# Kernel tuning notes

Hardware: AMD Instinct MI355X
Metric: run time of the kernel (lower is better)

Reference implementation:

```python
import jax, jax.numpy as jnp
import numpy as np

NEG_SLOPE = 0.2  # PyG GATConv default


def gat_conv(x, src, dst, W, att_src, att_dst, bias, n_nodes):
    # x: [N, F_in]; W: [F_in, H*C]; att_*: [H, C]; bias: [H*C]
    H, C = att_src.shape
    h = (x @ W).reshape(n_nodes, H, C)                      # [N, H, C]
    a_src = jnp.sum(h * att_src, axis=-1)                   # [N, H]
    a_dst = jnp.sum(h * att_dst, axis=-1)                   # [N, H]
    e = jax.nn.leaky_relu(a_src[src] + a_dst[dst], NEG_SLOPE)  # [E, H]
    # segment softmax over incoming edges of each dst node
    e_max = jax.ops.segment_max(e, dst, num_segments=n_nodes)
    e_max = jnp.where(jnp.isfinite(e_max), e_max, 0.0)
    ex = jnp.exp(e - e_max[dst])                             # [E, H]
    denom = jax.ops.segment_sum(ex, dst, num_segments=n_nodes)
    alpha = ex / (denom[dst] + 1e-16)                        # [E, H]
    msg = h[src] * alpha[:, :, None]                         # [E, H, C]
    out = jax.ops.segment_sum(msg, dst, num_segments=n_nodes)  # [N, H, C]
    return out.reshape(n_nodes, H * C) + bias


def setup_inputs() -> dict:
    key = jax.random.key(0)
    ks = jax.random.split(key, 12)
    N, F_in, Hd, heads, F_out, E = 50000, 128, 32, 8, 16, 800000
    x = jax.random.normal(ks[0], (N, F_in), dtype=jnp.float32)
    edge_index = jax.random.randint(ks[1], (2, E), 0, N, dtype=jnp.int64)
    g = 0.1
    return {
        "x": x,
        "edge_index": edge_index,
        "W1": jax.random.normal(ks[2], (F_in, heads * Hd), dtype=jnp.float32) * g,
        "att_src1": jax.random.normal(ks[3], (heads, Hd), dtype=jnp.float32) * g,
        "att_dst1": jax.random.normal(ks[4], (heads, Hd), dtype=jnp.float32) * g,
        "b1": jnp.zeros((heads * Hd,), dtype=jnp.float32),
        "W2": jax.random.normal(ks[5], (heads * Hd, Hd), dtype=jnp.float32) * g,
        "att_src2": jax.random.normal(ks[6], (1, Hd), dtype=jnp.float32) * g,
        "att_dst2": jax.random.normal(ks[7], (1, Hd), dtype=jnp.float32) * g,
        "b2": jnp.zeros((Hd,), dtype=jnp.float32),
        "Wout": jax.random.normal(ks[8], (Hd, F_out), dtype=jnp.float32) * g,
        "bout": jnp.zeros((F_out,), dtype=jnp.float32),
    }


def reference(x, edge_index, W1, att_src1, att_dst1, b1, W2, att_src2, att_dst2, b2, Wout, bout):
    N = x.shape[0]
    # PyG GATConv adds self loops by default
    loops = jnp.arange(N, dtype=edge_index.dtype)
    src = jnp.concatenate([edge_index[0], loops])
    dst = jnp.concatenate([edge_index[1], loops])
    h = jax.nn.elu(gat_conv(x, src, dst, W1, att_src1, att_dst1, b1, N))
    # dropout is identity in eval mode
    h = jax.nn.elu(gat_conv(h, src, dst, W2, att_src2, att_dst2, b2, N))
    return h @ Wout + bout
```

## Files before the change

kernel.cpp:

```cpp
#include <hip/hip_runtime.h>
#include <math.h>

#define NEG_SLOPE 0.2f

typedef __attribute__((ext_vector_type(8))) short bfrag8;
typedef __attribute__((ext_vector_type(4))) float f4acc;

__device__ __forceinline__ float bflo(unsigned int u) {
  union { unsigned int i; float f; } c;
  c.i = u << 16;
  return c.f;
}
__device__ __forceinline__ float bfhi(unsigned int u) {
  union { unsigned int i; float f; } c;
  c.i = u & 0xFFFF0000u;
  return c.f;
}
__device__ __forceinline__ unsigned short f2bf(float f) {
  union { float f; unsigned int i; } c;
  c.f = f;
  unsigned int i = c.i;
  return (unsigned short)((i + 0x7FFFu + ((i >> 16) & 1u)) >> 16);
}


__global__ __launch_bounds__(256) void hist_kernel(const int* __restrict__ ei,
                                                   int* __restrict__ counts, int e) {
  int i = blockIdx.x * 256 + threadIdx.x;
  if (i < e) atomicAdd(&counts[ei[e + i]], 1);
}

#define SCAN_TILE 2048
__global__ __launch_bounds__(256) void scan1_kernel(const int* __restrict__ counts,
                                                    int* __restrict__ offsets,
                                                    int* __restrict__ bsum, int n) {
  __shared__ int wtot[4];
  int tid = threadIdx.x;
  int base = blockIdx.x * SCAN_TILE + tid * 8;
  int v[8];
#pragma unroll
  for (int k = 0; k < 8; ++k) v[k] = (base + k < n) ? counts[base + k] + 1 : 0;
#pragma unroll
  for (int k = 1; k < 8; ++k) v[k] += v[k - 1];
  int tsum = v[7];
  int lane = tid & 63;
  int w = tid >> 6;
  int ws = tsum;
#pragma unroll
  for (int off = 1; off < 64; off <<= 1) {
    int t = __shfl_up(ws, off, 64);
    if (lane >= off) ws += t;
  }
  if (lane == 63) wtot[w] = ws;
  __syncthreads();
  int woff = 0;
#pragma unroll
  for (int k = 0; k < 3; ++k)
    if (k < w) woff += wtot[k];
  int thrBase = woff + ws - tsum;
#pragma unroll
  for (int k = 0; k < 8; ++k)
    if (base + k < n) offsets[base + k] = thrBase + v[k];
  if (tid == 255) bsum[blockIdx.x] = woff + ws;
}

__global__ __launch_bounds__(256) void scan3_kernel(const int* __restrict__ counts,
                                                    int* __restrict__ offsets,
                                                    const int* __restrict__ bsum,
                                                    int* __restrict__ cursor,
                                                    int n, int nb) {
  __shared__ int pres[64];
  int tid = threadIdx.x;
  if (tid < 64) {
    int v = (tid < nb) ? bsum[tid] : 0;
#pragma unroll
    for (int off = 1; off < 64; off <<= 1) {
      int t = __shfl_up(v, off, 64);
      if ((tid & 63) >= off) v += t;
    }
    pres[tid] = v;
  }
  __syncthreads();
  int i = blockIdx.x * 256 + tid;
  if (i > n) return;
  if (i == n) {
    offsets[n] = pres[nb - 1];
    return;
  }
  int b = i >> 11;
  int pre = (b == 0) ? 0 : pres[b - 1];
  int excl = pre + offsets[i] - (counts[i] + 1);
  offsets[i] = excl;
  cursor[i] = excl;
}

__global__ __launch_bounds__(256) void fill_kernel(const int* __restrict__ ei,
                                                   int* __restrict__ cursor,
                                                   int* __restrict__ csr, int n, int e) {
  int i = blockIdx.x * 256 + threadIdx.x;
  if (i < e) {
    int s = ei[i];
    int d = ei[e + i];
    int pos = atomicAdd(&cursor[d], 1);
    csr[pos] = s;
  } else if (i < e + n) {
    int node = i - e;
    int pos = atomicAdd(&cursor[node], 1);
    csr[pos] = node;
  } else if (i < e + n + 64) {
    csr[i] = 0;
  }
}


__global__ __launch_bounds__(256) void wcast_kernel(const float* __restrict__ W1,
                                                    const float* __restrict__ W2,
                                                    unsigned short* __restrict__ w1t,
                                                    unsigned short* __restrict__ w2t) {
  int gid = blockIdx.x * 256 + threadIdx.x;
#pragma unroll
  for (int u = 0; u < 4; ++u) {
    int j = gid * 4 + u;
    if (j < 128 * 256) {
      int k = j >> 8, c = j & 255;
      w1t[c * 128 + k] = f2bf(W1[j]);
    } else if (j < 128 * 256 + 256 * 32) {
      int j2 = j - 128 * 256;
      int k = j2 >> 5, c = j2 & 31;
      w2t[c * 256 + k] = f2bf(W2[j2]);
    }
  }
}

__global__ __launch_bounds__(256) void xcast_kernel(const float* __restrict__ x,
                                                    unsigned short* __restrict__ xb,
                                                    int total) {
  int gid = blockIdx.x * 256 + threadIdx.x;
  int i = gid * 8;
  if (i >= total) return;
  float4 v0 = *(const float4*)(x + i);
  float4 v1 = *(const float4*)(x + i + 4);
  uint4 q;
  q.x = (unsigned int)f2bf(v0.x) | ((unsigned int)f2bf(v0.y) << 16);
  q.y = (unsigned int)f2bf(v0.z) | ((unsigned int)f2bf(v0.w) << 16);
  q.z = (unsigned int)f2bf(v1.x) | ((unsigned int)f2bf(v1.y) << 16);
  q.w = (unsigned int)f2bf(v1.z) | ((unsigned int)f2bf(v1.w) << 16);
  *(uint4*)(xb + i) = q;
}


__global__ __launch_bounds__(256) void gemm1_kernel(const unsigned short* __restrict__ xb,
                                                    const unsigned short* __restrict__ w1t,
                                                    const float* __restrict__ att_src,
                                                    const float* __restrict__ att_dst,
                                                    unsigned short* __restrict__ h1b,
                                                    float* __restrict__ as1,
                                                    float* __restrict__ ad1, int n) {
  int tid = threadIdx.x;
  int wave = tid >> 6, lane = tid & 63;
  int quad = lane >> 4, l16 = lane & 15;
  int row0 = blockIdx.x * 64 + wave * 16;
  int col0 = blockIdx.y * 128;
  int rowA = min(row0 + l16, n - 1);

  f4acc acc[8];
#pragma unroll
  for (int t = 0; t < 8; ++t) acc[t] = (f4acc)(0.f);

#pragma unroll
  for (int kc = 0; kc < 4; ++kc) {
    bfrag8 a = *(const bfrag8*)(xb + (size_t)rowA * 128 + kc * 32 + quad * 8);
#pragma unroll
    for (int t = 0; t < 8; ++t) {
      bfrag8 b = *(const bfrag8*)(w1t + (size_t)(col0 + t * 16 + l16) * 128 + kc * 32 + quad * 8);
      acc[t] = __builtin_amdgcn_mfma_f32_16x16x32_bf16(a, b, acc[t], 0, 0, 0);
    }
  }

#pragma unroll
  for (int r = 0; r < 4; ++r) {
    int gr = row0 + quad * 4 + r;
    if (gr < n) {
#pragma unroll
      for (int t = 0; t < 8; ++t)
        h1b[(size_t)gr * 256 + col0 + t * 16 + l16] = f2bf(acc[t][r]);
    }
  }

  float s1[4][4], s2[4][4];
#pragma unroll
  for (int r = 0; r < 4; ++r)
#pragma unroll
    for (int hl = 0; hl < 4; ++hl) { s1[r][hl] = 0.f; s2[r][hl] = 0.f; }
#pragma unroll
  for (int t = 0; t < 8; ++t) {
    float av = att_src[col0 + t * 16 + l16];
    float dv = att_dst[col0 + t * 16 + l16];
    int hl = t >> 1;
#pragma unroll
    for (int r = 0; r < 4; ++r) {
      s1[r][hl] += acc[t][r] * av;
      s2[r][hl] += acc[t][r] * dv;
    }
  }
#pragma unroll
  for (int r = 0; r < 4; ++r) {
#pragma unroll
    for (int hl = 0; hl < 4; ++hl) {
      float v1 = s1[r][hl], v2 = s2[r][hl];
      v1 += __shfl_xor(v1, 1); v1 += __shfl_xor(v1, 2);
      v1 += __shfl_xor(v1, 4); v1 += __shfl_xor(v1, 8);
      v2 += __shfl_xor(v2, 1); v2 += __shfl_xor(v2, 2);
      v2 += __shfl_xor(v2, 4); v2 += __shfl_xor(v2, 8);
      if (l16 == 0) {
        int gr = row0 + quad * 4 + r;
        if (gr < n) {
          int hg = (col0 >> 5) + hl;
          as1[(size_t)gr * 8 + hg] = v1;
          ad1[(size_t)gr * 8 + hg] = v2;
        }
      }
    }
  }
}


__global__ __launch_bounds__(256) void agg1_kernel(const unsigned short* __restrict__ h1b,
                                                   const float* __restrict__ as1,
                                                   const float* __restrict__ ad1,
                                                   const int* __restrict__ offsets,
                                                   const int* __restrict__ csr,
                                                   const float* __restrict__ bias,
                                                   unsigned short* __restrict__ h1ob, int n) {
  __shared__ float peLds[4 * 64 * 8];
  int gtid = blockIdx.x * 256 + threadIdx.x;
  int node = gtid >> 6;
  int lane = gtid & 63;
  if (node >= n) return;
  float* myPe = peLds + (threadIdx.x >> 6) * 512;
  int beg = offsets[node], end = offsets[node + 1];
  int deg = end - beg;
  int half = lane >> 5, sub = lane & 31, head = sub >> 2;

  float4 adv0 = ((const float4*)(ad1 + (size_t)node * 8))[0];
  float4 adv1 = ((const float4*)(ad1 + (size_t)node * 8))[1];
  float ad_[8] = {adv0.x, adv0.y, adv0.z, adv0.w, adv1.x, adv1.y, adv1.z, adv1.w};

  float l = 0.f;
  float a[8] = {};

  for (int c0 = 0; c0 < deg; c0 += 64) {
    int cnt = min(64, deg - c0);
    bool valid = (c0 + lane) < deg;
    int s = csr[beg + c0 + lane];
    {
      const float4* ap = (const float4*)(as1 + (size_t)s * 8);
      float4 r0 = ap[0], r1 = ap[1];
      float asv[8] = {r0.x, r0.y, r0.z, r0.w, r1.x, r1.y, r1.z, r1.w};
      float pv[8];
#pragma unroll
      for (int h = 0; h < 8; ++h) {
        float ev = asv[h] + ad_[h];
        ev = ev > 0.f ? ev : NEG_SLOPE * ev;
        pv[h] = valid ? __expf(ev) : 0.f;
      }
      *(float4*)&myPe[lane * 8 + 0] = make_float4(pv[0], pv[1], pv[2], pv[3]);
      *(float4*)&myPe[lane * 8 + 4] = make_float4(pv[4], pv[5], pv[6], pv[7]);
    }
#pragma unroll 2
    for (int j = 0; j < cnt; j += 2) {
      int e = j + half;
      int s2 = csr[beg + c0 + e];
      float pe = myPe[e * 8 + head];
      l += pe;
      uint4 hv = *(const uint4*)(h1b + (size_t)s2 * 256 + sub * 8);
      a[0] += pe * bflo(hv.x);
      a[1] += pe * bfhi(hv.x);
      a[2] += pe * bflo(hv.y);
      a[3] += pe * bfhi(hv.y);
      a[4] += pe * bflo(hv.z);
      a[5] += pe * bfhi(hv.z);
      a[6] += pe * bflo(hv.w);
      a[7] += pe * bfhi(hv.w);
    }
  }
  l += __shfl_xor(l, 32);
#pragma unroll
  for (int i = 0; i < 8; ++i) a[i] += __shfl_xor(a[i], 32);

  if (half == 0) {
    float inv = 1.f / (l + 1e-16f);
    const float4* bp = (const float4*)(bias + sub * 8);
    float4 b0 = bp[0], b1 = bp[1];
    float o[8];
    o[0] = a[0] * inv + b0.x;
    o[1] = a[1] * inv + b0.y;
    o[2] = a[2] * inv + b0.z;
    o[3] = a[3] * inv + b0.w;
    o[4] = a[4] * inv + b1.x;
    o[5] = a[5] * inv + b1.y;
    o[6] = a[6] * inv + b1.z;
    o[7] = a[7] * inv + b1.w;
    unsigned int q[4];
#pragma unroll
    for (int j = 0; j < 4; ++j) {
      float e0 = o[j * 2], e1 = o[j * 2 + 1];
      e0 = e0 > 0.f ? e0 : expm1f(e0);
      e1 = e1 > 0.f ? e1 : expm1f(e1);
      q[j] = (unsigned int)f2bf(e0) | ((unsigned int)f2bf(e1) << 16);
    }
    *(uint4*)(h1ob + (size_t)node * 256 + sub * 8) = make_uint4(q[0], q[1], q[2], q[3]);
  }
}


__global__ __launch_bounds__(256) void gemm2_kernel(const unsigned short* __restrict__ h1ob,
                                                    const unsigned short* __restrict__ w2t,
                                                    const float* __restrict__ att_src,
                                                    const float* __restrict__ att_dst,
                                                    unsigned short* __restrict__ h2b,
                                                    float* __restrict__ as2,
                                                    float* __restrict__ ad2, int n) {
  int tid = threadIdx.x;
  int wave = tid >> 6, lane = tid & 63;
  int quad = lane >> 4, l16 = lane & 15;
  int row0 = blockIdx.x * 64 + wave * 16;
  int rowA = min(row0 + l16, n - 1);

  f4acc acc[2];
  acc[0] = (f4acc)(0.f);
  acc[1] = (f4acc)(0.f);

#pragma unroll
  for (int kc = 0; kc < 8; ++kc) {
    bfrag8 a = *(const bfrag8*)(h1ob + (size_t)rowA * 256 + kc * 32 + quad * 8);
#pragma unroll
    for (int t = 0; t < 2; ++t) {
      bfrag8 b = *(const bfrag8*)(w2t + (size_t)(t * 16 + l16) * 256 + kc * 32 + quad * 8);
      acc[t] = __builtin_amdgcn_mfma_f32_16x16x32_bf16(a, b, acc[t], 0, 0, 0);
    }
  }

#pragma unroll
  for (int r = 0; r < 4; ++r) {
    int gr = row0 + quad * 4 + r;
    if (gr < n) {
      h2b[(size_t)gr * 32 + l16] = f2bf(acc[0][r]);
      h2b[(size_t)gr * 32 + 16 + l16] = f2bf(acc[1][r]);
    }
  }

  float s1[4], s2v[4];
#pragma unroll
  for (int r = 0; r < 4; ++r) { s1[r] = 0.f; s2v[r] = 0.f; }
#pragma unroll
  for (int t = 0; t < 2; ++t) {
    float av = att_src[t * 16 + l16];
    float dv = att_dst[t * 16 + l16];
#pragma unroll
    for (int r = 0; r < 4; ++r) {
      s1[r] += acc[t][r] * av;
      s2v[r] += acc[t][r] * dv;
    }
  }
#pragma unroll
  for (int r = 0; r < 4; ++r) {
    float v1 = s1[r], v2 = s2v[r];
    v1 += __shfl_xor(v1, 1); v1 += __shfl_xor(v1, 2);
    v1 += __shfl_xor(v1, 4); v1 += __shfl_xor(v1, 8);
    v2 += __shfl_xor(v2, 1); v2 += __shfl_xor(v2, 2);
    v2 += __shfl_xor(v2, 4); v2 += __shfl_xor(v2, 8);
    if (l16 == 0) {
      int gr = row0 + quad * 4 + r;
      if (gr < n) {
        as2[gr] = v1;
        ad2[gr] = v2;
      }
    }
  }
}


__global__ __launch_bounds__(256) void agg2_kernel(const unsigned short* __restrict__ h2b,
                                                   const float* __restrict__ as2,
                                                   const float* __restrict__ ad2,
                                                   const int* __restrict__ offsets,
                                                   const int* __restrict__ csr,
                                                   const float* __restrict__ bias,
                                                   const float* __restrict__ Wout,
                                                   const float* __restrict__ bout,
                                                   float* __restrict__ out, int n) {
  __shared__ float peLds[4 * 64];
  __shared__ float wLds[512];
  __shared__ float hrow[4][32];
  int tid = threadIdx.x;
  wLds[tid] = Wout[tid];
  wLds[tid + 256] = Wout[tid + 256];
  __syncthreads();

  int gtid = blockIdx.x * 256 + tid;
  int node = gtid >> 6;
  int lane = gtid & 63;
  if (node >= n) return;
  int wv = tid >> 6;
  float* myPe = peLds + wv * 64;
  float ad = ad2[node];
  int beg = offsets[node], end = offsets[node + 1];
  int deg = end - beg;
  int quarter = lane >> 4;
  int dsub = lane & 15;

  float l = 0.f, a0 = 0.f, a1 = 0.f;
  for (int c0 = 0; c0 < deg; c0 += 64) {
    int cnt = min(64, deg - c0);
    bool valid = (c0 + lane) < deg;
    int s = csr[beg + c0 + lane];
    float ev = as2[s] + ad;
    ev = ev > 0.f ? ev : NEG_SLOPE * ev;
    myPe[lane] = valid ? __expf(ev) : 0.f;
#pragma unroll 2
    for (int j = 0; j < cnt; j += 4) {
      int e = j + quarter;
      int s2 = csr[beg + c0 + e];
      float pe = myPe[e];
      l += pe;
      unsigned int hv = *(const unsigned int*)(h2b + (size_t)s2 * 32 + dsub * 2);
      a0 += pe * bflo(hv);
      a1 += pe * bfhi(hv);
    }
  }
  l += __shfl_xor(l, 16);
  l += __shfl_xor(l, 32);
  a0 += __shfl_xor(a0, 16);
  a1 += __shfl_xor(a1, 16);
  a0 += __shfl_xor(a0, 32);
  a1 += __shfl_xor(a1, 32);
  if (lane < 16) {
    float inv = 1.f / (l + 1e-16f);
    float o0 = a0 * inv + bias[dsub * 2];
    float o1 = a1 * inv + bias[dsub * 2 + 1];
    o0 = o0 > 0.f ? o0 : expm1f(o0);
    o1 = o1 > 0.f ? o1 : expm1f(o1);
    hrow[wv][dsub * 2] = o0;
    hrow[wv][dsub * 2 + 1] = o1;
  }
  if (lane < 16) {
    float s = bout[lane];
#pragma unroll
    for (int c = 0; c < 32; ++c) s += hrow[wv][c] * wLds[c * 16 + lane];
    out[(size_t)node * 16 + lane] = s;
  }
}


extern "C" void kernel_launch(void* const* d_in, const int* in_sizes, int n_in,
                              void* d_out, int out_size, void* d_ws, size_t ws_size,
                              hipStream_t stream) {
  const float* x        = (const float*)d_in[0];
  const int*   ei       = (const int*)d_in[1];
  const float* W1       = (const float*)d_in[2];
  const float* att_src1 = (const float*)d_in[3];
  const float* att_dst1 = (const float*)d_in[4];
  const float* b1       = (const float*)d_in[5];
  const float* W2       = (const float*)d_in[6];
  const float* att_src2 = (const float*)d_in[7];
  const float* att_dst2 = (const float*)d_in[8];
  const float* b2       = (const float*)d_in[9];
  const float* Wout     = (const float*)d_in[10];
  const float* bout     = (const float*)d_in[11];
  float* out = (float*)d_out;

  int n = in_sizes[0] / 128;
  int e = in_sizes[1] / 2;

  char* w = (char*)d_ws;
  unsigned short* h1b  = (unsigned short*)w; w += (size_t)n * 256 * 2;
  unsigned short* h1ob = (unsigned short*)w; w += (size_t)n * 256 * 2;
  unsigned short* xb   = (unsigned short*)w; w += (size_t)n * 128 * 2;
  unsigned short* h2b  = (unsigned short*)w; w += (size_t)n * 32 * 2;
  unsigned short* w1t  = (unsigned short*)w; w += (size_t)256 * 128 * 2;
  unsigned short* w2t  = (unsigned short*)w; w += (size_t)32 * 256 * 2;
  float* as1  = (float*)w; w += (size_t)n * 8 * 4;
  float* ad1  = (float*)w; w += (size_t)n * 8 * 4;
  float* as2  = (float*)w; w += (size_t)n * 4;
  float* ad2  = (float*)w; w += (size_t)n * 4;
  int* counts  = (int*)w; w += (size_t)n * 4;
  int* offsets = (int*)w; w += (size_t)(n + 16) * 4;
  int* cursor  = (int*)w; w += (size_t)n * 4;
  int* csr     = (int*)w; w += (size_t)(e + n + 64) * 4;
  int* bsum    = (int*)w; w += (size_t)256 * 4;

  int nb = (n + SCAN_TILE - 1) / SCAN_TILE;

  hipMemsetAsync(counts, 0, (size_t)n * 4, stream);
  hist_kernel<<<(e + 255) / 256, 256, 0, stream>>>(ei, counts, e);
  scan1_kernel<<<nb, 256, 0, stream>>>(counts, offsets, bsum, n);
  scan3_kernel<<<(n + 256) / 256, 256, 0, stream>>>(counts, offsets, bsum, cursor, n, nb);
  fill_kernel<<<(e + n + 64 + 255) / 256, 256, 0, stream>>>(ei, cursor, csr, n, e);

  wcast_kernel<<<40, 256, 0, stream>>>(W1, W2, w1t, w2t);
  xcast_kernel<<<(n * 128 / 8 + 255) / 256, 256, 0, stream>>>(x, xb, n * 128);

  gemm1_kernel<<<dim3((n + 63) / 64, 2), 256, 0, stream>>>(xb, w1t, att_src1, att_dst1,
                                                           h1b, as1, ad1, n);
  agg1_kernel<<<(n + 3) / 4, 256, 0, stream>>>(h1b, as1, ad1, offsets, csr, b1, h1ob, n);

  gemm2_kernel<<<(n + 63) / 64, 256, 0, stream>>>(h1ob, w2t, att_src2, att_dst2,
                                                  h2b, as2, ad2, n);
  agg2_kernel<<<(n + 3) / 4, 256, 0, stream>>>(h2b, as2, ad2, offsets, csr, b2,
                                               Wout, bout, out, n);
}
```

Measured before the change: 342.7 us.

## Fuse histogram and scan into one last-block kernel, merge cast kernels

```diff
diff --git a/kernel.cpp b/kernel.cpp
--- a/kernel.cpp
+++ b/kernel.cpp
@@ -22,76 +22,59 @@
   unsigned int i = c.i;
   return (unsigned short)((i + 0x7FFFu + ((i >> 16) & 1u)) >> 16);
 }
-
-
-__global__ __launch_bounds__(256) void hist_kernel(const int* __restrict__ ei,
-                                                   int* __restrict__ counts, int e) {
-  int i = blockIdx.x * 256 + threadIdx.x;
+__device__ __forceinline__ float elu(float x) { return x > 0.f ? x : __expf(x) - 1.f; }
+
+
+__global__ __launch_bounds__(1024) void histscan_kernel(const int* __restrict__ ei,
+                                                        int* __restrict__ counts,
+                                                        int* __restrict__ done,
+                                                        int* __restrict__ offsets,
+                                                        int* __restrict__ cursor,
+                                                        int n, int e) {
+  int i = blockIdx.x * 1024 + threadIdx.x;
   if (i < e) atomicAdd(&counts[ei[e + i]], 1);
-}
-
-#define SCAN_TILE 2048
-__global__ __launch_bounds__(256) void scan1_kernel(const int* __restrict__ counts,
-                                                    int* __restrict__ offsets,
-                                                    int* __restrict__ bsum, int n) {
-  __shared__ int wtot[4];
+  __threadfence();
+  __syncthreads();
+  __shared__ int lastFlag;
+  if (threadIdx.x == 0) lastFlag = (atomicAdd(done, 1) == (int)gridDim.x - 1);
+  __syncthreads();
+  if (!lastFlag) return;
+  __threadfence();
+
+  const volatile int* cv = counts;
+  __shared__ int tileOff;
+  __shared__ int wsum[16];
   int tid = threadIdx.x;
-  int base = blockIdx.x * SCAN_TILE + tid * 8;
-  int v[8];
-#pragma unroll
-  for (int k = 0; k < 8; ++k) v[k] = (base + k < n) ? counts[base + k] + 1 : 0;
-#pragma unroll
-  for (int k = 1; k < 8; ++k) v[k] += v[k - 1];
-  int tsum = v[7];
-  int lane = tid & 63;
-  int w = tid >> 6;
-  int ws = tsum;
-#pragma unroll
-  for (int off = 1; off < 64; off <<= 1) {
-    int t = __shfl_up(ws, off, 64);
-    if (lane >= off) ws += t;
-  }
-  if (lane == 63) wtot[w] = ws;
+  if (tid == 0) tileOff = 0;
   __syncthreads();
-  int woff = 0;
-#pragma unroll
-  for (int k = 0; k < 3; ++k)
-    if (k < w) woff += wtot[k];
-  int thrBase = woff + ws - tsum;
-#pragma unroll
-  for (int k = 0; k < 8; ++k)
-    if (base + k < n) offsets[base + k] = thrBase + v[k];
-  if (tid == 255) bsum[blockIdx.x] = woff + ws;
-}
-
-__global__ __launch_bounds__(256) void scan3_kernel(const int* __restrict__ counts,
-                                                    int* __restrict__ offsets,
-                                                    const int* __restrict__ bsum,
-                                                    int* __restrict__ cursor,
-                                                    int n, int nb) {
-  __shared__ int pres[64];
-  int tid = threadIdx.x;
-  if (tid < 64) {
-    int v = (tid < nb) ? bsum[tid] : 0;
+  int nt = (n + 1023) >> 10;
+  int lane = tid & 63, wv = tid >> 6;
+  for (int tb = 0; tb < nt; ++tb) {
+    int idx = tb * 1024 + tid;
+    int v = (idx < n) ? cv[idx] + 1 : 0;
+    int ws = v;
 #pragma unroll
     for (int off = 1; off < 64; off <<= 1) {
-      int t = __shfl_up(v, off, 64);
-      if ((tid & 63) >= off) v += t;
-    }
-    pres[tid] = v;
-  }
-  __syncthreads();
-  int i = blockIdx.x * 256 + tid;
-  if (i > n) return;
-  if (i == n) {
-    offsets[n] = pres[nb - 1];
-    return;
-  }
-  int b = i >> 11;
-  int pre = (b == 0) ? 0 : pres[b - 1];
-  int excl = pre + offsets[i] - (counts[i] + 1);
-  offsets[i] = excl;
-  cursor[i] = excl;
+      int t = __shfl_up(ws, off, 64);
+      if (lane >= off) ws += t;
+    }
+    if (lane == 63) wsum[wv] = ws;
+    __syncthreads();
+    int woff = 0;
+#pragma unroll
+    for (int k = 0; k < 15; ++k)
+      if (k < wv) woff += wsum[k];
+    int incl = woff + ws;
+    int excl = tileOff + incl - v;
+    if (idx < n) {
+      offsets[idx] = excl;
+      cursor[idx] = excl;
+    }
+    __syncthreads();
+    if (tid == 1023) tileOff += incl;
+    __syncthreads();
+  }
+  if (tid == 0) offsets[n] = tileOff;
 }
 
 __global__ __launch_bounds__(256) void fill_kernel(const int* __restrict__ ei,
@@ -113,14 +96,31 @@
 }
 
 
-__global__ __launch_bounds__(256) void wcast_kernel(const float* __restrict__ W1,
-                                                    const float* __restrict__ W2,
-                                                    unsigned short* __restrict__ w1t,
-                                                    unsigned short* __restrict__ w2t) {
+__global__ __launch_bounds__(256) void cast_kernel(const float* __restrict__ x,
+                                                   const float* __restrict__ W1,
+                                                   const float* __restrict__ W2,
+                                                   unsigned short* __restrict__ xb,
+                                                   unsigned short* __restrict__ w1t,
+                                                   unsigned short* __restrict__ w2t,
+                                                   int xThreads, int totalx) {
   int gid = blockIdx.x * 256 + threadIdx.x;
+  if (gid < xThreads) {
+    int i = gid * 8;
+    if (i >= totalx) return;
+    float4 v0 = *(const float4*)(x + i);
+    float4 v1 = *(const float4*)(x + i + 4);
+    uint4 q;
+    q.x = (unsigned int)f2bf(v0.x) | ((unsigned int)f2bf(v0.y) << 16);
+    q.y = (unsigned int)f2bf(v0.z) | ((unsigned int)f2bf(v0.w) << 16);
+    q.z = (unsigned int)f2bf(v1.x) | ((unsigned int)f2bf(v1.y) << 16);
+    q.w = (unsigned int)f2bf(v1.z) | ((unsigned int)f2bf(v1.w) << 16);
+    *(uint4*)(xb + i) = q;
+    return;
+  }
+  int g2 = gid - xThreads;
 #pragma unroll
   for (int u = 0; u < 4; ++u) {
-    int j = gid * 4 + u;
+    int j = g2 * 4 + u;
     if (j < 128 * 256) {
       int k = j >> 8, c = j & 255;
       w1t[c * 128 + k] = f2bf(W1[j]);
@@ -130,22 +130,6 @@
       w2t[c * 256 + k] = f2bf(W2[j2]);
     }
   }
-}
-
-__global__ __launch_bounds__(256) void xcast_kernel(const float* __restrict__ x,
-                                                    unsigned short* __restrict__ xb,
-                                                    int total) {
-  int gid = blockIdx.x * 256 + threadIdx.x;
-  int i = gid * 8;
-  if (i >= total) return;
-  float4 v0 = *(const float4*)(x + i);
-  float4 v1 = *(const float4*)(x + i + 4);
-  uint4 q;
-  q.x = (unsigned int)f2bf(v0.x) | ((unsigned int)f2bf(v0.y) << 16);
-  q.y = (unsigned int)f2bf(v0.z) | ((unsigned int)f2bf(v0.w) << 16);
-  q.z = (unsigned int)f2bf(v1.x) | ((unsigned int)f2bf(v1.y) << 16);
-  q.w = (unsigned int)f2bf(v1.z) | ((unsigned int)f2bf(v1.w) << 16);
-  *(uint4*)(xb + i) = q;
 }
 
 
@@ -267,7 +251,7 @@
       *(float4*)&myPe[lane * 8 + 0] = make_float4(pv[0], pv[1], pv[2], pv[3]);
       *(float4*)&myPe[lane * 8 + 4] = make_float4(pv[4], pv[5], pv[6], pv[7]);
     }
-#pragma unroll 2
+#pragma unroll 4
     for (int j = 0; j < cnt; j += 2) {
       int e = j + half;
       int s2 = csr[beg + c0 + e];
@@ -293,22 +277,18 @@
     const float4* bp = (const float4*)(bias + sub * 8);
     float4 b0 = bp[0], b1 = bp[1];
     float o[8];
-    o[0] = a[0] * inv + b0.x;
-    o[1] = a[1] * inv + b0.y;
-    o[2] = a[2] * inv + b0.z;
-    o[3] = a[3] * inv + b0.w;
-    o[4] = a[4] * inv + b1.x;
-    o[5] = a[5] * inv + b1.y;
-    o[6] = a[6] * inv + b1.z;
-    o[7] = a[7] * inv + b1.w;
+    o[0] = elu(a[0] * inv + b0.x);
+    o[1] = elu(a[1] * inv + b0.y);
+    o[2] = elu(a[2] * inv + b0.z);
+    o[3] = elu(a[3] * inv + b0.w);
+    o[4] = elu(a[4] * inv + b1.x);
+    o[5] = elu(a[5] * inv + b1.y);
+    o[6] = elu(a[6] * inv + b1.z);
+    o[7] = elu(a[7] * inv + b1.w);
     unsigned int q[4];
 #pragma unroll
-    for (int j = 0; j < 4; ++j) {
-      float e0 = o[j * 2], e1 = o[j * 2 + 1];
-      e0 = e0 > 0.f ? e0 : expm1f(e0);
-      e1 = e1 > 0.f ? e1 : expm1f(e1);
-      q[j] = (unsigned int)f2bf(e0) | ((unsigned int)f2bf(e1) << 16);
-    }
+    for (int j = 0; j < 4; ++j)
+      q[j] = (unsigned int)f2bf(o[j * 2]) | ((unsigned int)f2bf(o[j * 2 + 1]) << 16);
     *(uint4*)(h1ob + (size_t)node * 256 + sub * 8) = make_uint4(q[0], q[1], q[2], q[3]);
   }
 }
@@ -418,7 +398,7 @@
     float ev = as2[s] + ad;
     ev = ev > 0.f ? ev : NEG_SLOPE * ev;
     myPe[lane] = valid ? __expf(ev) : 0.f;
-#pragma unroll 2
+#pragma unroll 4
     for (int j = 0; j < cnt; j += 4) {
       int e = j + quarter;
       int s2 = csr[beg + c0 + e];
@@ -437,10 +417,8 @@
   a1 += __shfl_xor(a1, 32);
   if (lane < 16) {
     float inv = 1.f / (l + 1e-16f);
-    float o0 = a0 * inv + bias[dsub * 2];
-    float o1 = a1 * inv + bias[dsub * 2 + 1];
-    o0 = o0 > 0.f ? o0 : expm1f(o0);
-    o1 = o1 > 0.f ? o1 : expm1f(o1);
+    float o0 = elu(a0 * inv + bias[dsub * 2]);
+    float o1 = elu(a1 * inv + bias[dsub * 2 + 1]);
     hrow[wv][dsub * 2] = o0;
     hrow[wv][dsub * 2 + 1] = o1;
   }
@@ -485,21 +463,20 @@
   float* as2  = (float*)w; w += (size_t)n * 4;
   float* ad2  = (float*)w; w += (size_t)n * 4;
   int* counts  = (int*)w; w += (size_t)n * 4;
+  int* done    = (int*)w; w += (size_t)16 * 4;
   int* offsets = (int*)w; w += (size_t)(n + 16) * 4;
   int* cursor  = (int*)w; w += (size_t)n * 4;
   int* csr     = (int*)w; w += (size_t)(e + n + 64) * 4;
-  int* bsum    = (int*)w; w += (size_t)256 * 4;
-
-  int nb = (n + SCAN_TILE - 1) / SCAN_TILE;
-
-  hipMemsetAsync(counts, 0, (size_t)n * 4, stream);
-  hist_kernel<<<(e + 255) / 256, 256, 0, stream>>>(ei, counts, e);
-  scan1_kernel<<<nb, 256, 0, stream>>>(counts, offsets, bsum, n);
-  scan3_kernel<<<(n + 256) / 256, 256, 0, stream>>>(counts, offsets, bsum, cursor, n, nb);
+
+  hipMemsetAsync(counts, 0, (size_t)(n + 16) * 4, stream);
+  int nbh = (e + 1023) / 1024;
+  histscan_kernel<<<nbh, 1024, 0, stream>>>(ei, counts, done, offsets, cursor, n, e);
   fill_kernel<<<(e + n + 64 + 255) / 256, 256, 0, stream>>>(ei, cursor, csr, n, e);
 
-  wcast_kernel<<<40, 256, 0, stream>>>(W1, W2, w1t, w2t);
-  xcast_kernel<<<(n * 128 / 8 + 255) / 256, 256, 0, stream>>>(x, xb, n * 128);
+  int xThreads = (n * 128 + 7) / 8;
+  int castThreads = xThreads + (128 * 256 + 256 * 32 + 3) / 4;
+  cast_kernel<<<(castThreads + 255) / 256, 256, 0, stream>>>(x, W1, W2, xb, w1t, w2t,
+                                                             xThreads, n * 128);
 
   gemm1_kernel<<<dim3((n + 63) / 64, 2), 256, 0, stream>>>(xb, w1t, att_src1, att_dst1,
                                                            h1b, as1, ad1, n);
```

Result: slower. 539.3 us (+57.4%).
